# Kernel optimization log

Hardware: AMD Instinct MI355X
Metric: run time of the kernel (lower is better)

Reference implementation:

```python
import jax, jax.numpy as jnp
from jax import lax
import numpy as np

B = 16
C1, H1, W1 = 512, 28, 28   # wide_resnet50_2 layer2 @ 224px
C2, H2, W2 = 1024, 14, 14  # wide_resnet50_2 layer3 @ 224px
M = 15000                  # memory bank max size (embedding_max_len)
D = C1 + C2                # 1536
IMG = 224                  # input_size
NUM_NEIGHBORS = 9
SIGMA = 4.0                # anomalib AnomalyMapGenerator default
KS = 2 * int(4.0 * SIGMA + 0.5) + 1  # 33 (kornia kernel-size rule)


def setup_inputs() -> dict:
    key = jax.random.key(0)
    k1, k2, k3 = jax.random.split(key, 3)
    return {
        "feat1": jax.random.normal(k1, (B, C1, H1, W1), dtype=jnp.float32),
        "feat2": jax.random.normal(k2, (B, C2, H2, W2), dtype=jnp.float32),
        "memory_bank": jax.random.normal(k3, (M, D), dtype=jnp.float32),
    }


def _avg_pool3(x):
    # torch.nn.AvgPool2d(3, 1, 1) with count_include_pad=True -> sum window / 9
    s = lax.reduce_window(x, 0.0, lax.add, (1, 1, 3, 3), (1, 1, 1, 1),
                          [(0, 0), (0, 0), (1, 1), (1, 1)])
    return s / 9.0


def _edist(x, y):
    x_norm = jnp.sum(x * x, axis=-1, keepdims=True)
    y_norm = jnp.sum(y * y, axis=-1, keepdims=True)
    res = x_norm - 2.0 * jnp.matmul(x, jnp.swapaxes(y, -2, -1)) + jnp.swapaxes(y_norm, -2, -1)
    return jnp.sqrt(jnp.maximum(res, 0.0))


def _gauss_kernel():
    t = jnp.arange(KS, dtype=jnp.float32) - (KS - 1) / 2.0
    g = jnp.exp(-(t * t) / (2.0 * SIGMA * SIGMA))
    return g / jnp.sum(g)


def _gaussian_blur(x):
    # separable depthwise gaussian blur with reflect padding (kornia GaussianBlur2d)
    g = _gauss_kernel()
    p = KS // 2
    x = jnp.pad(x, ((0, 0), (0, 0), (p, p), (p, p)), mode='reflect')
    dn = ('NCHW', 'OIHW', 'NCHW')
    x = lax.conv_general_dilated(x, g.reshape(1, 1, KS, 1), (1, 1), 'VALID', dimension_numbers=dn)
    x = lax.conv_general_dilated(x, g.reshape(1, 1, 1, KS), (1, 1), 'VALID', dimension_numbers=dn)
    return x


def reference(feat1, feat2, memory_bank):
    # 1. feature pooling + hierarchical embedding concat
    f1 = _avg_pool3(feat1)                                   # [B,512,28,28]
    f2 = _avg_pool3(feat2)                                   # [B,1024,14,14]
    f2 = jax.image.resize(f2, (f2.shape[0], f2.shape[1], H1, W1), 'bilinear')
    emb = jnp.concatenate([f1, f2], axis=1)                  # [B,1536,28,28]
    b, d = emb.shape[0], emb.shape[1]
    e = emb.transpose(0, 2, 3, 1).reshape(-1, d)             # [B*P, D]

    # 2. brute-force 1-NN against memory bank
    dist = _edist(e, memory_bank)                            # [N, M]
    patch_scores = jnp.min(dist, axis=1)                     # [N]
    locations = jnp.argmin(dist, axis=1)                     # [N]
    P = H1 * W1
    ps = patch_scores.reshape(b, P)
    loc = locations.reshape(b, P)

    # 3. image-level anomaly score with num_neighbors=9 re-weighting
    bidx = jnp.arange(b)
    mp = jnp.argmax(ps, axis=1)                              # [B]
    max_feat = e.reshape(b, P, d)[bidx, mp]                  # [B,D]
    score = ps[bidx, mp]                                     # [B]
    nn_index = loc[bidx, mp]                                 # [B]
    nn_sample = memory_bank[nn_index]                        # [B,D]
    d_nb = _edist(nn_sample, memory_bank)                    # [B,M]
    _, support = lax.top_k(-d_nb, NUM_NEIGHBORS)             # [B,9] smallest
    sup_feats = memory_bank[support]                         # [B,9,D]
    d2 = _edist(max_feat[:, None, :], sup_feats)             # [B,1,9]
    weights = (1.0 - jax.nn.softmax(d2[:, 0, :], axis=1))[:, 0]
    pred_score = weights * score                             # [B]

    # 4. anomaly map: upsample patch scores to input size + gaussian blur
    amap = ps.reshape(b, 1, H1, W1)
    amap = jax.image.resize(amap, (b, 1, IMG, IMG), 'bilinear')
    amap = _gaussian_blur(amap)                              # [B,1,224,224]
    return amap, pred_score
```

## Files before the change

kernel.cpp:

```cpp
#include <hip/hip_runtime.h>
#include <stdint.h>

#define B_    16
#define C1_   512
#define C2_   1024
#define H2_   14
#define D_    1536
#define K16_  96
#define P_    784
#define N_    12544
#define M_    15000
#define MPAD_ 15104
#define MT1_  118
#define MT2_  59
#define NT_   98
#define IMG_  224
#define KS_   33

typedef unsigned short u16;
typedef unsigned int   u32;
typedef unsigned long long u64;

__device__ __forceinline__ u16 f2bf(float x) {
    u32 u = __float_as_uint(x);
    u = u + 0x7fffu + ((u >> 16) & 1u);
    return (u16)(u >> 16);
}
__device__ __forceinline__ float bf2f(u16 h) {
    return __uint_as_float(((u32)h) << 16);
}
__device__ __forceinline__ u32 ordf(float f) {
    u32 u = __float_as_uint(f);
    return (u & 0x80000000u) ? ~u : (u | 0x80000000u);
}
__device__ __forceinline__ float unordf(u32 o) {
    u32 u = (o & 0x80000000u) ? (o ^ 0x80000000u) : ~o;
    return __uint_as_float(u);
}


__global__ void k_pool2(const float* __restrict__ feat2, float* __restrict__ pooled2) {
    int idx = blockIdx.x * 256 + threadIdx.x;
    if (idx >= B_ * C2_ * H2_ * H2_) return;
    int x = idx % 14, y = (idx / 14) % 14, bc = idx / 196;
    const float* src = feat2 + (size_t)bc * 196;
    float s = 0.f;
    for (int dy = -1; dy <= 1; ++dy) {
        int yy = y + dy; if (yy < 0 || yy > 13) continue;
        for (int dx = -1; dx <= 1; ++dx) {
            int xx = x + dx; if (xx < 0 || xx > 13) continue;
            s += src[yy * 14 + xx];
        }
    }
    pooled2[idx] = s * (1.f / 9.f);
}

__global__ __launch_bounds__(192)
void k_bank(const float* __restrict__ bank, u16* __restrict__ Bph,
            u16* __restrict__ Bpl, float* __restrict__ ynorm) {
    int m = blockIdx.x, tid = threadIdx.x;
    float nrm = 0.f;
    float v[8];
    if (m < M_) {
        const float4* src = (const float4*)(bank + (size_t)m * D_ + tid * 8);
        float4 a = src[0], b = src[1];
        v[0]=a.x; v[1]=a.y; v[2]=a.z; v[3]=a.w; v[4]=b.x; v[5]=b.y; v[6]=b.z; v[7]=b.w;
#pragma unroll
        for (int i = 0; i < 8; ++i) nrm += v[i] * v[i];
    } else {
#pragma unroll
        for (int i = 0; i < 8; ++i) v[i] = 0.f;
    }
    u32 hw[4], lw[4];
#pragma unroll
    for (int i = 0; i < 4; ++i) {
        u16 h0 = f2bf(v[2*i]),   l0 = f2bf(v[2*i]   - bf2f(h0));
        u16 h1 = f2bf(v[2*i+1]), l1 = f2bf(v[2*i+1] - bf2f(h1));
        hw[i] = (u32)h0 | ((u32)h1 << 16);
        lw[i] = (u32)l0 | ((u32)l1 << 16);
    }
    int c = tid * 8;
    int k16 = c >> 4, kh = (c >> 3) & 1;
    int mt2 = m >> 8, r = m & 255, gb = r >> 5, rA = r & 31;
    size_t off = ((((size_t)mt2 * K16_ + k16) * 8 + gb) * 64 + kh * 32 + rA) * 8;
    *(uint4*)(Bph + off) = make_uint4(hw[0], hw[1], hw[2], hw[3]);
    *(uint4*)(Bpl + off) = make_uint4(lw[0], lw[1], lw[2], lw[3]);
    __shared__ float red[3];
    for (int offr = 32; offr; offr >>= 1) nrm += __shfl_down(nrm, offr, 64);
    int wave = tid >> 6, lane = tid & 63;
    if (lane == 0) red[wave] = nrm;
    __syncthreads();
    if (tid == 0) {
        float t = red[0] + red[1] + red[2];
        ynorm[m] = (m < M_) ? t : __uint_as_float(0x7f800000u);
    }
}

__device__ __forceinline__ void emb_store(u16* Ah, u16* Al, u16* Aph,
                                          int n, int col, float v) {
    u16 h = f2bf(v);
    size_t off = (size_t)n * D_ + col;
    Ah[off] = h; Al[off] = f2bf(v - bf2f(h));
    int pt = n >> 7, r = n & 127, g = r >> 5, rA = r & 31;
    int k16 = col >> 4, kh = (col >> 3) & 1, j = col & 7;
    Aph[((((size_t)pt * K16_ + k16) * 4 + g) * 64 + kh * 32 + rA) * 8 + j] = h;
}

__global__ __launch_bounds__(256)
void k_embed(const float* __restrict__ feat1, const float* __restrict__ pooled2,
             u16* __restrict__ Ah, u16* __restrict__ Al, u16* __restrict__ Aph,
             float* __restrict__ xnorm) {
    __shared__ float sF[3 * 64 * 29];
    __shared__ float xn[28];
    const int tid = threadIdx.x, lane = tid & 63, wave = tid >> 6;
    const int b = blockIdx.x / 28, y = blockIdx.x % 28;
    const int brow = b * P_ + y * 28;
    if (tid < 28) xn[tid] = 0.f;

    float sy = y * 0.5f - 0.25f;
    int iy = (int)floorf(sy);
    float fy = sy - iy;
    int y0 = min(max(iy, 0), 13), y1 = min(max(iy + 1, 0), 13);
    __syncthreads();

    for (int cc = 0; cc < 8; ++cc) {
        for (int j = tid; j < 3 * 64 * 28; j += 256) {
            int x = j % 28, c = (j / 28) % 64, r = j / (28 * 64);
            int yy = y - 1 + r;
            float v = 0.f;
            if (yy >= 0 && yy < 28)
                v = feat1[((size_t)(b * C1_ + cc * 64 + c)) * 784 + yy * 28 + x];
            sF[(r * 64 + c) * 29 + x] = v;
        }
        __syncthreads();
        for (int it = 0; it < 7; ++it) {
            int x = it * 4 + wave, c = lane;
            float s = 0.f;
#pragma unroll
            for (int r = 0; r < 3; ++r) {
                int base = (r * 64 + c) * 29;
                if (x > 0) s += sF[base + x - 1];
                s += sF[base + x];
                if (x < 27) s += sF[base + x + 1];
            }
            float v = s * (1.f / 9.f);
            emb_store(Ah, Al, Aph, brow + x, cc * 64 + c, v);
            float vv = v * v;
            for (int m = 1; m < 64; m <<= 1) vv += __shfl_xor(vv, m, 64);
            if (lane == 0) atomicAdd(&xn[x], vv);
        }
        __syncthreads();
    }

    for (int cc = 0; cc < 16; ++cc) {
        for (int it = 0; it < 7; ++it) {
            int x = it * 4 + wave, c = lane;
            const float* sp = pooled2 + ((size_t)(b * C2_ + cc * 64 + c)) * 196;
            float sx = x * 0.5f - 0.25f;
            int ix = (int)floorf(sx);
            float fx = sx - ix;
            int x0 = min(max(ix, 0), 13), x1 = min(max(ix + 1, 0), 13);
            float v = (1.f - fy) * ((1.f - fx) * sp[y0 * 14 + x0] + fx * sp[y0 * 14 + x1])
                    + fy * ((1.f - fx) * sp[y1 * 14 + x0] + fx * sp[y1 * 14 + x1]);
            emb_store(Ah, Al, Aph, brow + x, C1_ + cc * 64 + c, v);
            float vv = v * v;
            for (int m = 1; m < 64; m <<= 1) vv += __shfl_xor(vv, m, 64);
            if (lane == 0) atomicAdd(&xn[x], vv);
        }
    }
    __syncthreads();
    if (tid < 28) xnorm[brow + tid] = xn[tid];
}

typedef __bf16 bf16x8 __attribute__((ext_vector_type(8)));
typedef float  f32x16 __attribute__((ext_vector_type(16)));

__global__ __launch_bounds__(256, 2)
void k_gemm1(const u16* __restrict__ Aph, const u16* __restrict__ Bph,
             const float* __restrict__ ynorm, float* __restrict__ partf) {
    __shared__ float smin[128][2];
    const int tid = threadIdx.x, lane = tid & 63, wave = tid >> 6;
    const int GM = 4, nig = GM * NT_;
    const int grp = blockIdx.x / nig, rem = blockIdx.x - grp * nig;
    const int first = grp * GM;
    const int gsz = (MT2_ - first) < GM ? (MT2_ - first) : GM;
    const int mt = first + rem % gsz;
    const int pt = rem / gsz;
    const int p0 = pt * 128, m0 = mt * 256;

    f32x16 acc[2][4];
#pragma unroll
    for (int i = 0; i < 2; ++i)
#pragma unroll
        for (int j = 0; j < 4; ++j)
#pragma unroll
            for (int e = 0; e < 16; ++e) acc[i][j][e] = 0.f;

    const int wr = (wave >> 1) * 64, wc = (wave & 1) * 128;
    const u16* aB = Aph + ((size_t)pt * K16_ * 4 + (wr >> 5)) * 512 + lane * 8;
    const u16* bB = Bph + ((size_t)mt * K16_ * 8 + (wc >> 5)) * 512 + lane * 8;

#pragma unroll 4
    for (int k16 = 0; k16 < K16_; ++k16) {
        bf16x8 af[2], bfr[4];
        const u16* ak = aB + (size_t)k16 * 4 * 512;
        const u16* bk = bB + (size_t)k16 * 8 * 512;
        af[0]  = *(const bf16x8*)(ak);
        af[1]  = *(const bf16x8*)(ak + 512);
        bfr[0] = *(const bf16x8*)(bk);
        bfr[1] = *(const bf16x8*)(bk + 512);
        bfr[2] = *(const bf16x8*)(bk + 1024);
        bfr[3] = *(const bf16x8*)(bk + 1536);
#pragma unroll
        for (int ti = 0; ti < 2; ++ti)
#pragma unroll
            for (int tj = 0; tj < 4; ++tj)
                acc[ti][tj] = __builtin_amdgcn_mfma_f32_32x32x16_bf16(
                    af[ti], bfr[tj], acc[ti][tj], 0, 0, 0);
    }

    const int c32 = lane & 31, kh = lane >> 5;
    float yn[4];
#pragma unroll
    for (int tj = 0; tj < 4; ++tj) yn[tj] = ynorm[m0 + wc + tj * 32 + c32];
#pragma unroll
    for (int ti = 0; ti < 2; ++ti) {
#pragma unroll
        for (int reg = 0; reg < 16; ++reg) {
            const int rloc = wr + ti * 32 + (reg & 3) + 8 * (reg >> 2) + 4 * kh;
            float v = __uint_as_float(0x7f800000u);
#pragma unroll
            for (int tj = 0; tj < 4; ++tj)
                v = fminf(v, yn[tj] - 2.0f * acc[ti][tj][reg]);
#pragma unroll
            for (int msk = 1; msk < 32; msk <<= 1)
                v = fminf(v, __shfl_xor(v, msk, 64));
            if (c32 == 0) smin[rloc][wave & 1] = v;
        }
    }
    __syncthreads();
    if (tid < 128)
        partf[(size_t)mt * N_ + p0 + tid] = fminf(smin[tid][0], smin[tid][1]);
}

__global__ void k_reduce(const float* __restrict__ partf, const float* __restrict__ xnorm,
                         float* __restrict__ ps) {
    int n = blockIdx.x * 128 + threadIdx.x;
    float best = __uint_as_float(0x7f800000u);
    for (int t = 0; t < MT2_; ++t)
        best = fminf(best, partf[(size_t)t * N_ + n]);
    ps[n] = sqrtf(fmaxf(best + xnorm[n], 0.f));
}

__global__ void k_cand(const float* __restrict__ ps, int* __restrict__ candrow) {
    int b = blockIdx.x, tid = threadIdx.x;
    __shared__ u64 red[4];
    u64 prev = ~0ull;
    for (int j = 0; j < 8; ++j) {
        u64 best = 0;
        for (int p = tid; p < P_; p += 256) {
            u64 pk = ((u64)ordf(ps[b * P_ + p]) << 32) | (u32)(~(u32)p);
            if (pk < prev && pk > best) best = pk;
        }
        for (int msk = 1; msk < 64; msk <<= 1) {
            u64 o = __shfl_xor(best, msk, 64);
            best = o > best ? o : best;
        }
        int wave = tid >> 6, lane = tid & 63;
        if (lane == 0) red[wave] = best;
        __syncthreads();
        u64 m = red[0];
        for (int w = 1; w < 4; ++w) m = red[w] > m ? red[w] : m;
        if (tid == 0) candrow[b * 8 + j] = b * P_ + (int)(~(u32)m);
        prev = m;
        __syncthreads();
    }
}

#define GLD16(dst, src) __builtin_amdgcn_global_load_lds( \
    (const __attribute__((address_space(1))) void*)(src), \
    (__attribute__((address_space(3))) void*)(dst), 16, 0, 0)

__global__ __launch_bounds__(256)
void k_gexact(const u16* __restrict__ Ah, const u16* __restrict__ Al,
              const u16* __restrict__ Bph, const u16* __restrict__ Bpl,
              const int* __restrict__ candrow, float* __restrict__ pdot) {
    __shared__ u16 sA[2][128 * 32];
    __shared__ int scand[128];

    const int tid = threadIdx.x;
    const int lane = tid & 63, wave = tid >> 6;
    const int mt = blockIdx.x, slice = blockIdx.y;
    if (tid < 128) scand[tid] = candrow[tid];

    f32x16 acc[2][2];
#pragma unroll
    for (int i = 0; i < 2; ++i)
#pragma unroll
        for (int j = 0; j < 2; ++j)
#pragma unroll
            for (int e = 0; e < 16; ++e) acc[i][j][e] = 0.f;

    const int srow = lane >> 2;
    const int scol = ((lane & 3) ^ ((lane >> 3) & 3)) * 8;
    const int wr = (wave >> 1) * 64, wc = (wave & 1) * 64;
    const int rA = lane & 31;
    const int sw = (lane >> 1) & 3;
    const size_t bbase = (((size_t)(mt >> 1) * K16_) * 8 + (mt & 1) * 4 + (wc >> 5)) * 512 + lane * 8;
    __syncthreads();

    for (int kt = slice * 12; kt < slice * 12 + 12; ++kt) {
        const int k0 = kt * 32;
#pragma unroll
        for (int s = 0; s < 2; ++s) {
            const int slab = wave * 2 + s;
            const int row = slab * 16 + srow;
            const int grow = scand[row];
            GLD16(&sA[0][slab * 512], Ah + (size_t)grow * D_ + k0 + scol);
            GLD16(&sA[1][slab * 512], Al + (size_t)grow * D_ + k0 + scol);
        }
        __syncthreads();
#pragma unroll
        for (int ks = 0; ks < 2; ++ks) {
            const int co = ((ks * 2 + (lane >> 5)) ^ sw) * 8;
            const size_t bo = bbase + (size_t)(kt * 2 + ks) * 8 * 512;
            bf16x8 ah0 = *(const bf16x8*)&sA[0][(wr + rA) * 32 + co];
            bf16x8 ah1 = *(const bf16x8*)&sA[0][(wr + 32 + rA) * 32 + co];
            bf16x8 al0 = *(const bf16x8*)&sA[1][(wr + rA) * 32 + co];
            bf16x8 al1 = *(const bf16x8*)&sA[1][(wr + 32 + rA) * 32 + co];
            bf16x8 bh0 = *(const bf16x8*)(Bph + bo);
            bf16x8 bh1 = *(const bf16x8*)(Bph + bo + 512);
            bf16x8 bl0 = *(const bf16x8*)(Bpl + bo);
            bf16x8 bl1 = *(const bf16x8*)(Bpl + bo + 512);
            acc[0][0] = __builtin_amdgcn_mfma_f32_32x32x16_bf16(ah0, bh0, acc[0][0], 0, 0, 0);
            acc[0][1] = __builtin_amdgcn_mfma_f32_32x32x16_bf16(ah0, bh1, acc[0][1], 0, 0, 0);
            acc[1][0] = __builtin_amdgcn_mfma_f32_32x32x16_bf16(ah1, bh0, acc[1][0], 0, 0, 0);
            acc[1][1] = __builtin_amdgcn_mfma_f32_32x32x16_bf16(ah1, bh1, acc[1][1], 0, 0, 0);
            acc[0][0] = __builtin_amdgcn_mfma_f32_32x32x16_bf16(ah0, bl0, acc[0][0], 0, 0, 0);
            acc[0][1] = __builtin_amdgcn_mfma_f32_32x32x16_bf16(ah0, bl1, acc[0][1], 0, 0, 0);
            acc[1][0] = __builtin_amdgcn_mfma_f32_32x32x16_bf16(ah1, bl0, acc[1][0], 0, 0, 0);
            acc[1][1] = __builtin_amdgcn_mfma_f32_32x32x16_bf16(ah1, bl1, acc[1][1], 0, 0, 0);
            acc[0][0] = __builtin_amdgcn_mfma_f32_32x32x16_bf16(al0, bh0, acc[0][0], 0, 0, 0);
            acc[0][1] = __builtin_amdgcn_mfma_f32_32x32x16_bf16(al0, bh1, acc[0][1], 0, 0, 0);
            acc[1][0] = __builtin_amdgcn_mfma_f32_32x32x16_bf16(al1, bh0, acc[1][0], 0, 0, 0);
            acc[1][1] = __builtin_amdgcn_mfma_f32_32x32x16_bf16(al1, bh1, acc[1][1], 0, 0, 0);
        }
        __syncthreads();
    }

    const int wrB = wave >> 1, wcB = wave & 1;
    const int half = lane >> 5, c32 = lane & 31;
    float* base = pdot + ((size_t)(slice * MT1_ + mt) * 128) * 128;
#pragma unroll
    for (int ti = 0; ti < 2; ++ti) {
#pragma unroll
        for (int reg = 0; reg < 16; ++reg) {
            const int rloc = wrB * 64 + ti * 32 + 4 * half + (reg & 3) + 8 * (reg >> 2);
#pragma unroll
            for (int tj = 0; tj < 2; ++tj)
                base[(size_t)rloc * 128 + wcB * 64 + tj * 32 + c32] = acc[ti][tj][reg];
        }
    }
}

__global__ void k_pickc(const float* __restrict__ pdot, const float* __restrict__ ynorm,
                        u64* __restrict__ candmin) {
    int i = blockIdx.x, tid = threadIdx.x;
    __shared__ u64 red[4];
    u64 best = ~0ull;
    for (int m = tid; m < MPAD_; m += 256) {
        float dot = 0.f;
#pragma unroll
        for (int s = 0; s < 4; ++s)
            dot += pdot[((size_t)(s * MT1_ + (m >> 7)) * 128 + i) * 128 + (m & 127)];
        float v = ynorm[m] - 2.f * dot;
        u64 pk = ((u64)ordf(v) << 32) | (u32)m;
        best = pk < best ? pk : best;
    }
    for (int msk = 1; msk < 64; msk <<= 1) {
        u64 o = __shfl_xor(best, msk, 64);
        best = o < best ? o : best;
    }
    int wave = tid >> 6, lane = tid & 63;
    if (lane == 0) red[wave] = best;
    __syncthreads();
    if (tid == 0) {
        u64 m = red[0];
        for (int w = 1; w < 4; ++w) m = red[w] < m ? red[w] : m;
        candmin[i] = m;
    }
}

__global__ void k_pick(const u64* __restrict__ candmin, const float* __restrict__ xnorm,
                       const int* __restrict__ candrow, int* __restrict__ mprow,
                       int* __restrict__ nnidx, float* __restrict__ score) {
    __shared__ float sps[128];
    __shared__ int sloc[128];
    int i = threadIdx.x;
    u64 best = candmin[i];
    float val = unordf((u32)(best >> 32)) + xnorm[candrow[i]];
    sps[i] = sqrtf(fmaxf(val, 0.f));
    sloc[i] = (int)(u32)best;
    __syncthreads();
    if (i < B_) {
        float bs = -1.f; int bj = 0; int brw = 1 << 30;
        for (int j = 0; j < 8; ++j) {
            int idx = i * 8 + j;
            float v = sps[idx];
            int row = candrow[idx];
            if (v > bs || (v == bs && row < brw)) { bs = v; bj = idx; brw = row; }
        }
        mprow[i] = brw;
        nnidx[i] = sloc[bj];
        score[i] = bs;
    }
}

__global__ void k_dnb(const float* __restrict__ bank, const float* __restrict__ ynorm,
                      const int* __restrict__ nnidx, float* __restrict__ dnb) {
    int wave = threadIdx.x >> 6, lane = threadIdx.x & 63;
    int m = blockIdx.x * 4 + wave;
    if (m >= M_) return;
    const float4* br = (const float4*)(bank + (size_t)m * D_);
    float acc[B_];
#pragma unroll
    for (int b = 0; b < B_; ++b) acc[b] = 0.f;
#pragma unroll
    for (int p = 0; p < 6; ++p) {
        float4 c = br[p * 64 + lane];
#pragma unroll
        for (int b = 0; b < B_; ++b) {
            const float4* nr = (const float4*)(bank + (size_t)nnidx[b] * D_);
            float4 a = nr[p * 64 + lane];
            acc[b] += a.x * c.x + a.y * c.y + a.z * c.z + a.w * c.w;
        }
    }
    float ym = ynorm[m];
    float keep = 0.f;
#pragma unroll
    for (int b = 0; b < B_; ++b) {
        float v = acc[b];
        for (int msk = 1; msk < 64; msk <<= 1) v += __shfl_xor(v, msk, 64);
        if (lane == b) keep = v;
    }
    if (lane < B_) {
        float ynn = ynorm[nnidx[lane]];
        dnb[lane * M_ + m] = sqrtf(fmaxf(ynn - 2.f * keep + ym, 0.f));
    }
}

__global__ void k_top9a(const float* __restrict__ dnb, u64* __restrict__ cand9) {
    int blk = blockIdx.x;
    int b = blk >> 3, ch = blk & 7;
    int base = ch * 1875;
    int tid = threadIdx.x;
    __shared__ u64 red[4];
    u64 prev = 0;
    for (int p = 0; p < 9; ++p) {
        u64 best = ~0ull;
        for (int i = tid; i < 1875; i += 256) {
            float v = dnb[b * M_ + base + i];
            u64 pk = ((u64)ordf(v) << 32) | (u32)(base + i);
            if (pk > prev && pk < best) best = pk;
        }
        for (int msk = 1; msk < 64; msk <<= 1) {
            u64 o = __shfl_xor(best, msk, 64);
            best = o < best ? o : best;
        }
        int wave = tid >> 6, lane = tid & 63;
        if (lane == 0) red[wave] = best;
        __syncthreads();
        u64 m = red[0];
        for (int w = 1; w < 4; ++w) m = red[w] < m ? red[w] : m;
        if (tid == 0) cand9[blk * 9 + p] = m;
        prev = m;
        __syncthreads();
    }
}
__global__ void k_top9b(const u64* __restrict__ cand9, int* __restrict__ support) {
    int b = blockIdx.x, lane = threadIdx.x;
    u64 v0 = lane < 72 ? cand9[b * 72 + lane] : ~0ull;
    u64 v1 = (lane + 64) < 72 ? cand9[b * 72 + lane + 64] : ~0ull;
    u64 prev = 0;
    for (int p = 0; p < 9; ++p) {
        u64 best = ~0ull;
        if (v0 > prev && v0 < best) best = v0;
        if (v1 > prev && v1 < best) best = v1;
        for (int msk = 1; msk < 64; msk <<= 1) {
            u64 o = __shfl_xor(best, msk, 64);
            best = o < best ? o : best;
        }
        if (lane == 0) support[b * 9 + p] = (int)(u32)best;
        prev = best;
    }
}

__global__ void k_final(const u16* __restrict__ Ah, const u16* __restrict__ Al,
                        const float* __restrict__ bank, const float* __restrict__ ynorm,
                        const float* __restrict__ xnorm, const int* __restrict__ mprow,
                        const int* __restrict__ support, const float* __restrict__ score,
                        float* __restrict__ out_score) {
    int b = blockIdx.x;
    int wave = threadIdx.x >> 6, lane = threadIdx.x & 63;
    __shared__ float d2s[9];
    int row = mprow[b];
    float xn = xnorm[row];
    for (int s = wave; s < 9; s += 4) {
        int sup = support[b * 9 + s];
        float acc = 0.f;
        for (int p = 0; p < 24; ++p) {
            int k = p * 64 + lane;
            float e = bf2f(Ah[(size_t)row * D_ + k]) + bf2f(Al[(size_t)row * D_ + k]);
            acc += e * bank[(size_t)sup * D_ + k];
        }
        for (int msk = 1; msk < 64; msk <<= 1) acc += __shfl_xor(acc, msk, 64);
        if (lane == 0) d2s[s] = sqrtf(fmaxf(xn - 2.f * acc + ynorm[sup], 0.f));
    }
    __syncthreads();
    if (threadIdx.x == 0) {
        float mx = d2s[0];
        for (int i = 1; i < 9; ++i) mx = fmaxf(mx, d2s[i]);
        float den = 0.f;
        for (int i = 0; i < 9; ++i) den += expf(d2s[i] - mx);
        float w = 1.f - expf(d2s[0] - mx) / den;
        out_score[b] = w * score[b];
    }
}

__global__ void k_upsample(const float* __restrict__ ps, float* __restrict__ U) {
    int idx = blockIdx.x * 256 + threadIdx.x;
    if (idx >= B_ * IMG_ * IMG_) return;
    int x = idx % IMG_, y = (idx / IMG_) % IMG_, b = idx / (IMG_ * IMG_);
    float sx = x * 0.125f - 0.4375f, sy = y * 0.125f - 0.4375f;
    int ix = (int)floorf(sx), iy = (int)floorf(sy);
    float fx = sx - ix, fy = sy - iy;
    int x0 = min(max(ix, 0), 27), x1 = min(max(ix + 1, 0), 27);
    int y0 = min(max(iy, 0), 27), y1 = min(max(iy + 1, 0), 27);
    const float* p = ps + b * P_;
    U[idx] = (1.f - fy) * ((1.f - fx) * p[y0 * 28 + x0] + fx * p[y0 * 28 + x1])
           + fy * ((1.f - fx) * p[y1 * 28 + x0] + fx * p[y1 * 28 + x1]);
}

__global__ void k_blurh(const float* __restrict__ U, float* __restrict__ T) {
    __shared__ float g[KS_];
    __shared__ float gs;
    int tid = threadIdx.x;
    if (tid < KS_) { float d = tid - 16.f; g[tid] = expf(-(d * d) / 32.0f); }
    __syncthreads();
    if (tid == 0) { float s = 0.f; for (int i = 0; i < KS_; ++i) s += g[i]; gs = 1.f / s; }
    __syncthreads();
    int idx = blockIdx.x * 256 + tid;
    if (idx >= B_ * IMG_ * IMG_) return;
    int x = idx % IMG_, rowbase = idx - x;
    float a = 0.f;
    for (int t = 0; t < KS_; ++t) {
        int xx = x + t - 16;
        xx = xx < 0 ? -xx : (xx > 223 ? 446 - xx : xx);
        a += g[t] * U[rowbase + xx];
    }
    T[idx] = a * gs;
}
__global__ void k_blurv(const float* __restrict__ T, float* __restrict__ out) {
    __shared__ float g[KS_];
    __shared__ float gs;
    int tid = threadIdx.x;
    if (tid < KS_) { float d = tid - 16.f; g[tid] = expf(-(d * d) / 32.0f); }
    __syncthreads();
    if (tid == 0) { float s = 0.f; for (int i = 0; i < KS_; ++i) s += g[i]; gs = 1.f / s; }
    __syncthreads();
    int idx = blockIdx.x * 256 + tid;
    if (idx >= B_ * IMG_ * IMG_) return;
    int x = idx % IMG_, y = (idx / IMG_) % IMG_, b = idx / (IMG_ * IMG_);
    float a = 0.f;
    for (int t = 0; t < KS_; ++t) {
        int yy = y + t - 16;
        yy = yy < 0 ? -yy : (yy > 223 ? 446 - yy : yy);
        a += g[t] * T[(b * IMG_ + yy) * IMG_ + x];
    }
    out[idx] = a * gs;
}

extern "C" void kernel_launch(void* const* d_in, const int* in_sizes, int n_in,
                              void* d_out, int out_size, void* d_ws, size_t ws_size,
                              hipStream_t stream) {
    const float* feat1 = (const float*)d_in[0];
    const float* feat2 = (const float*)d_in[1];
    const float* bank  = (const float*)d_in[2];
    float* out = (float*)d_out;
    char* ws = (char*)d_ws;

    const size_t apack_sz = (size_t)NT_ * K16_ * 4 * 512 * 2;
    const size_t bpack_sz = (size_t)MT2_ * K16_ * 8 * 512 * 2;

    size_t o = 0;
    u16* Ah  = (u16*)(ws + o); o += (size_t)N_ * D_ * 2;
    u16* Al  = (u16*)(ws + o); o += (size_t)N_ * D_ * 2;
    size_t o_Ap = o;
    u16* Aph = (u16*)(ws + o); o += apack_sz;
    size_t o_Bp = o;
    u16* Bph = (u16*)(ws + o); o += bpack_sz;
    u16* Bpl = (u16*)(ws + o); o += bpack_sz;
    size_t o_scr = o;
    float* pooled2 = (float*)(ws + o_scr);
    float* partf   = (float*)(ws + o_scr);
    size_t r1 = (size_t)MT2_ * N_ * 4, r2 = (size_t)B_ * C2_ * 196 * 4;
    o += (r1 > r2 ? r1 : r2);
    float* xnorm = (float*)(ws + o); o += (size_t)N_ * 4;
    float* ynorm = (float*)(ws + o); o += (size_t)MPAD_ * 4;
    float* ps    = (float*)(ws + o); o += (size_t)N_ * 4;
    int* candrow = (int*)(ws + o);   o += 512;
    u64* candmin = (u64*)(ws + o);   o += 128 * 8;
    float* dnb   = (float*)(ws + o); o += (size_t)B_ * M_ * 4;
    u64* cand9   = (u64*)(ws + o);   o += 128 * 9 * 8;
    int*   mprow = (int*)(ws + o);   o += 64;
    int*   nnidx = (int*)(ws + o);   o += 64;
    float* score = (float*)(ws + o); o += 64;
    int* support = (int*)(ws + o);   o += 9 * B_ * 4;
    float* pdot  = (float*)(ws + o_Ap);
    float* U = (float*)(ws + o_Bp);
    float* T = (float*)(ws + o_Bp + (size_t)B_ * IMG_ * IMG_ * 4);

    k_pool2<<<(B_ * C2_ * H2_ * H2_ + 255) / 256, 256, 0, stream>>>(feat2, pooled2);
    k_bank<<<MPAD_, 192, 0, stream>>>(bank, Bph, Bpl, ynorm);
    k_embed<<<B_ * 28, 256, 0, stream>>>(feat1, pooled2, Ah, Al, Aph, xnorm);
    k_gemm1<<<MT2_ * NT_, 256, 0, stream>>>(Aph, Bph, ynorm, partf);
    k_reduce<<<NT_, 128, 0, stream>>>(partf, xnorm, ps);
    k_cand<<<B_, 256, 0, stream>>>(ps, candrow);
    k_gexact<<<dim3(MT1_, 4), 256, 0, stream>>>(Ah, Al, Bph, Bpl, candrow, pdot);
    k_pickc<<<128, 256, 0, stream>>>(pdot, ynorm, candmin);
    k_pick<<<1, 128, 0, stream>>>(candmin, xnorm, candrow, mprow, nnidx, score);
    k_dnb<<<(M_ + 3) / 4, 256, 0, stream>>>(bank, ynorm, nnidx, dnb);
    k_top9a<<<128, 256, 0, stream>>>(dnb, cand9);
    k_top9b<<<B_, 64, 0, stream>>>(cand9, support);
    k_final<<<B_, 256, 0, stream>>>(Ah, Al, bank, ynorm, xnorm, mprow, support, score,
                                    out + (size_t)B_ * IMG_ * IMG_);
    k_upsample<<<(B_ * IMG_ * IMG_ + 255) / 256, 256, 0, stream>>>(ps, U);
    k_blurh<<<(B_ * IMG_ * IMG_ + 255) / 256, 256, 0, stream>>>(U, T);
    k_blurv<<<(B_ * IMG_ * IMG_ + 255) / 256, 256, 0, stream>>>(T, out);
}
```

Measured before the change: 1.253 ms.

## Vectorize embedding stores and double-buffer register fragments in GEMM1

The embedding kernel now has each thread compute 8 consecutive channels and write them with 16-byte vector stores to the hi/lo and packed layouts. This replaces the scattered 2-byte stores and the per-element wave shuffle reductions, at the cost of idling 32 of 256 threads. The GEMM1 main loop now prefetches fragments for the next k-steps into a second register set while MFMAs run on the current set. This is meant to hide global load latency, in exchange for higher register pressure.

Result: faster. 1.192 ms (-4.9%).

```diff
diff --git a/kernel.cpp b/kernel.cpp
--- a/kernel.cpp
+++ b/kernel.cpp
@@ -96,14 +96,24 @@
     }
 }
 
-__device__ __forceinline__ void emb_store(u16* Ah, u16* Al, u16* Aph,
-                                          int n, int col, float v) {
-    u16 h = f2bf(v);
-    size_t off = (size_t)n * D_ + col;
-    Ah[off] = h; Al[off] = f2bf(v - bf2f(h));
+__device__ __forceinline__ void store8(u16* __restrict__ Ah, u16* __restrict__ Al,
+                                       u16* __restrict__ Aph, int n, int colb,
+                                       const float* v) {
+    u32 hw[4], lw[4];
+#pragma unroll
+    for (int i = 0; i < 4; ++i) {
+        u16 h0 = f2bf(v[2*i]),   l0 = f2bf(v[2*i]   - bf2f(h0));
+        u16 h1 = f2bf(v[2*i+1]), l1 = f2bf(v[2*i+1] - bf2f(h1));
+        hw[i] = (u32)h0 | ((u32)h1 << 16);
+        lw[i] = (u32)l0 | ((u32)l1 << 16);
+    }
+    size_t off = (size_t)n * D_ + colb;
+    *(uint4*)(Ah + off) = make_uint4(hw[0], hw[1], hw[2], hw[3]);
+    *(uint4*)(Al + off) = make_uint4(lw[0], lw[1], lw[2], lw[3]);
     int pt = n >> 7, r = n & 127, g = r >> 5, rA = r & 31;
-    int k16 = col >> 4, kh = (col >> 3) & 1, j = col & 7;
-    Aph[((((size_t)pt * K16_ + k16) * 4 + g) * 64 + kh * 32 + rA) * 8 + j] = h;
+    int k16 = colb >> 4, kh = (colb >> 3) & 1;
+    size_t poff = ((((size_t)pt * K16_ + k16) * 4 + g) * 64 + kh * 32 + rA) * 8;
+    *(uint4*)(Aph + poff) = make_uint4(hw[0], hw[1], hw[2], hw[3]);
 }
 
 __global__ __launch_bounds__(256)
@@ -112,10 +122,12 @@
              float* __restrict__ xnorm) {
     __shared__ float sF[3 * 64 * 29];
     __shared__ float xn[28];
-    const int tid = threadIdx.x, lane = tid & 63, wave = tid >> 6;
+    const int tid = threadIdx.x;
     const int b = blockIdx.x / 28, y = blockIdx.x % 28;
     const int brow = b * P_ + y * 28;
     if (tid < 28) xn[tid] = 0.f;
+    const int x = tid >> 3, oct = tid & 7;
+    const bool act = tid < 224;
 
     float sy = y * 0.5f - 0.25f;
     int iy = (int)floorf(sy);
@@ -125,47 +137,53 @@
 
     for (int cc = 0; cc < 8; ++cc) {
         for (int j = tid; j < 3 * 64 * 28; j += 256) {
-            int x = j % 28, c = (j / 28) % 64, r = j / (28 * 64);
+            int xx = j % 28, c = (j / 28) % 64, r = j / (28 * 64);
             int yy = y - 1 + r;
             float v = 0.f;
             if (yy >= 0 && yy < 28)
-                v = feat1[((size_t)(b * C1_ + cc * 64 + c)) * 784 + yy * 28 + x];
-            sF[(r * 64 + c) * 29 + x] = v;
-        }
-        __syncthreads();
-        for (int it = 0; it < 7; ++it) {
-            int x = it * 4 + wave, c = lane;
-            float s = 0.f;
-#pragma unroll
-            for (int r = 0; r < 3; ++r) {
-                int base = (r * 64 + c) * 29;
-                if (x > 0) s += sF[base + x - 1];
-                s += sF[base + x];
-                if (x < 27) s += sF[base + x + 1];
+                v = feat1[((size_t)(b * C1_ + cc * 64 + c)) * 784 + yy * 28 + xx];
+            sF[(r * 64 + c) * 29 + xx] = v;
+        }
+        __syncthreads();
+        if (act) {
+            float v[8]; float nrm = 0.f;
+#pragma unroll
+            for (int j = 0; j < 8; ++j) {
+                int c = oct * 8 + j;
+                float s = 0.f;
+#pragma unroll
+                for (int r = 0; r < 3; ++r) {
+                    int base = (r * 64 + c) * 29;
+                    if (x > 0) s += sF[base + x - 1];
+                    s += sF[base + x];
+                    if (x < 27) s += sF[base + x + 1];
+                }
+                v[j] = s * (1.f / 9.f);
+                nrm += v[j] * v[j];
             }
-            float v = s * (1.f / 9.f);
-            emb_store(Ah, Al, Aph, brow + x, cc * 64 + c, v);
-            float vv = v * v;
-            for (int m = 1; m < 64; m <<= 1) vv += __shfl_xor(vv, m, 64);
-            if (lane == 0) atomicAdd(&xn[x], vv);
-        }
-        __syncthreads();
-    }
-
+            store8(Ah, Al, Aph, brow + x, cc * 64 + oct * 8, v);
+            atomicAdd(&xn[x], nrm);
+        }
+        __syncthreads();
+    }
+
+    float sx = x * 0.5f - 0.25f;
+    int ix = (int)floorf(sx);
+    float fx = sx - ix;
+    int x0 = min(max(ix, 0), 13), x1 = min(max(ix + 1, 0), 13);
     for (int cc = 0; cc < 16; ++cc) {
-        for (int it = 0; it < 7; ++it) {
-            int x = it * 4 + wave, c = lane;
-            const float* sp = pooled2 + ((size_t)(b * C2_ + cc * 64 + c)) * 196;
-            float sx = x * 0.5f - 0.25f;
-            int ix = (int)floorf(sx);
-            float fx = sx - ix;
-            int x0 = min(max(ix, 0), 13), x1 = min(max(ix + 1, 0), 13);
-            float v = (1.f - fy) * ((1.f - fx) * sp[y0 * 14 + x0] + fx * sp[y0 * 14 + x1])
-                    + fy * ((1.f - fx) * sp[y1 * 14 + x0] + fx * sp[y1 * 14 + x1]);
-            emb_store(Ah, Al, Aph, brow + x, C1_ + cc * 64 + c, v);
-            float vv = v * v;
-            for (int m = 1; m < 64; m <<= 1) vv += __shfl_xor(vv, m, 64);
-            if (lane == 0) atomicAdd(&xn[x], vv);
+        if (act) {
+            float v[8]; float nrm = 0.f;
+#pragma unroll
+            for (int j = 0; j < 8; ++j) {
+                int c = cc * 64 + oct * 8 + j;
+                const float* sp = pooled2 + ((size_t)(b * C2_ + c)) * 196;
+                float vv = (1.f - fy) * ((1.f - fx) * sp[y0 * 14 + x0] + fx * sp[y0 * 14 + x1])
+                         + fy * ((1.f - fx) * sp[y1 * 14 + x0] + fx * sp[y1 * 14 + x1]);
+                v[j] = vv; nrm += vv * vv;
+            }
+            store8(Ah, Al, Aph, brow + x, C1_ + cc * 64 + oct * 8, v);
+            atomicAdd(&xn[x], nrm);
         }
     }
     __syncthreads();
@@ -197,27 +215,34 @@
             for (int e = 0; e < 16; ++e) acc[i][j][e] = 0.f;
 
     const int wr = (wave >> 1) * 64, wc = (wave & 1) * 128;
-    const u16* aB = Aph + ((size_t)pt * K16_ * 4 + (wr >> 5)) * 512 + lane * 8;
-    const u16* bB = Bph + ((size_t)mt * K16_ * 8 + (wc >> 5)) * 512 + lane * 8;
-
-#pragma unroll 4
-    for (int k16 = 0; k16 < K16_; ++k16) {
-        bf16x8 af[2], bfr[4];
-        const u16* ak = aB + (size_t)k16 * 4 * 512;
-        const u16* bk = bB + (size_t)k16 * 8 * 512;
-        af[0]  = *(const bf16x8*)(ak);
-        af[1]  = *(const bf16x8*)(ak + 512);
-        bfr[0] = *(const bf16x8*)(bk);
-        bfr[1] = *(const bf16x8*)(bk + 512);
-        bfr[2] = *(const bf16x8*)(bk + 1024);
-        bfr[3] = *(const bf16x8*)(bk + 1536);
-#pragma unroll
-        for (int ti = 0; ti < 2; ++ti)
-#pragma unroll
-            for (int tj = 0; tj < 4; ++tj)
-                acc[ti][tj] = __builtin_amdgcn_mfma_f32_32x32x16_bf16(
-                    af[ti], bfr[tj], acc[ti][tj], 0, 0, 0);
-    }
+    const u16* ap = Aph + ((size_t)pt * K16_ * 4 + (wr >> 5)) * 512 + lane * 8;
+    const u16* bp = Bph + ((size_t)mt * K16_ * 8 + (wc >> 5)) * 512 + lane * 8;
+
+    bf16x8 af[2][2], bfr[2][4];
+#define LOADSET(s) do { \
+    af[s][0]  = *(const bf16x8*)(ap); \
+    af[s][1]  = *(const bf16x8*)(ap + 512); \
+    bfr[s][0] = *(const bf16x8*)(bp); \
+    bfr[s][1] = *(const bf16x8*)(bp + 512); \
+    bfr[s][2] = *(const bf16x8*)(bp + 1024); \
+    bfr[s][3] = *(const bf16x8*)(bp + 1536); \
+    ap += 2048; bp += 4096; } while (0)
+#define MFMASET(s) do { \
+    _Pragma("unroll") \
+    for (int ti = 0; ti < 2; ++ti) \
+        _Pragma("unroll") \
+        for (int tj = 0; tj < 4; ++tj) \
+            acc[ti][tj] = __builtin_amdgcn_mfma_f32_32x32x16_bf16( \
+                af[s][ti], bfr[s][tj], acc[ti][tj], 0, 0, 0); } while (0)
+
+    LOADSET(0); LOADSET(1);
+    for (int k = 0; k < 47; ++k) {
+        MFMASET(0); LOADSET(0);
+        MFMASET(1); LOADSET(1);
+    }
+    MFMASET(0); MFMASET(1);
+#undef LOADSET
+#undef MFMASET
 
     const int c32 = lane & 31, kh = lane >> 5;
     float yn[4];
```
